# Optimization experiments

Hardware: AMD Instinct MI355X
Metric: run time of the kernel (lower is better)

## Reference

```python
import jax, jax.numpy as jnp
import numpy as np

B = 16384        # batch
P = 8            # num policies (experts)
D = 512          # latent dim
A = 64           # action dim
H = 1024         # hidden dim


def setup_inputs() -> dict:
    key = jax.random.key(0)
    ks = jax.random.split(key, 7)
    latents = jax.random.normal(ks[0], (B, D), dtype=jnp.float32)
    actions = jax.random.normal(ks[1], (B, A), dtype=jnp.float32)
    policy_indices = jax.random.randint(ks[2], (B,), 0, P, dtype=jnp.int64)
    # Per-policy 2-layer MLP params: concat(latent, action) -> hidden -> latent
    scale1 = 1.0 / np.sqrt(D + A)
    scale2 = 1.0 / np.sqrt(H)
    W1 = jax.random.normal(ks[3], (P, D + A, H), dtype=jnp.float32) * scale1
    b1 = jnp.zeros((P, H), dtype=jnp.float32)
    W2 = jax.random.normal(ks[4], (P, H, D), dtype=jnp.float32) * scale2
    b2 = jnp.zeros((P, D), dtype=jnp.float32)
    return {"latents": latents, "actions": actions, "policy_indices": policy_indices,
            "W1": W1, "b1": b1, "W2": W2, "b2": b2}


def reference(latents, actions, policy_indices, W1, b1, W2, b2):
    # Original: for each policy i, route rows with policy_indices == i through
    # that policy's dynamics model; scatter results back into next_latents.
    # Equivalent dense form: run all experts, then select per-row expert output.
    x = jnp.concatenate([latents, actions], axis=-1)          # [B, D+A]
    h = jax.nn.relu(jnp.einsum('bd,pdh->bph', x, W1) + b1)    # [B, P, H]
    y = jnp.einsum('bph,phd->bpd', h, W2) + b2                # [B, P, D]
    idx = policy_indices[:, None, None]                       # [B, 1, 1]
    next_latents = jnp.take_along_axis(y, idx, axis=1)[:, 0]  # [B, D]
    return next_latents
```

## Files before the change

kernel.cpp:

```cpp
#include <hip/hip_runtime.h>
#include <hip/hip_bf16.h>
#include <stdint.h>

#define B_SZ 16384
#define P_SZ 8
#define D_SZ 512
#define A_SZ 64
#define K1 576
#define H_SZ 1024
#define NSEG 64
#define MB_MAX 72
#define BPAD (B_SZ + P_SZ*256)
#define PREP_BLOCKS (BPAD * 72 / 256)
#define TR1_BLOCKS (P_SZ * 9 * 16)
#define TR2_BLOCKS (P_SZ * 16 * 8)
#define G1_GRID (BPAD / 128 * (H_SZ / 64))
#define G2_GRID (BPAD / 128 * (D_SZ / 64))

typedef __bf16 bf16_t;
typedef __bf16 bf16x8 __attribute__((ext_vector_type(8)));
typedef float f32x4 __attribute__((ext_vector_type(4)));

__device__ __forceinline__ void glds16(const void* g, void* l) {
    __builtin_amdgcn_global_load_lds(
        (const __attribute__((address_space(1))) unsigned*)g,
        (__attribute__((address_space(3))) unsigned*)l, 16, 0, 0);
}


__global__ __launch_bounds__(256) void hist_block(const int* __restrict__ pol,
                                                  int* __restrict__ blockhist,
                                                  int* __restrict__ rowidx) {
    __shared__ int lc[P_SZ];
    int t = threadIdx.x;
    if (t < P_SZ) lc[t] = 0;
    __syncthreads();
    int gid = blockIdx.x * 256 + t;
    rowidx[gid] = -1;
    if (gid < BPAD - B_SZ) rowidx[B_SZ + gid] = -1;
    atomicAdd(&lc[pol[gid]], 1);
    __syncthreads();
    if (t < P_SZ) blockhist[blockIdx.x * P_SZ + t] = lc[t];
}

__global__ __launch_bounds__(256) void prefix_kernel(const int* __restrict__ blockhist,
                                                     int* __restrict__ counts,
                                                     int* __restrict__ cursors,
                                                     int* __restrict__ blk_p) {
    __shared__ int csh[P_SZ];
    int t = threadIdx.x;
    int p = t >> 5, i = t & 31;
    int s = blockhist[i * P_SZ + p] + blockhist[(i + 32) * P_SZ + p];
#pragma unroll
    for (int m = 16; m >= 1; m >>= 1) s += __shfl_xor(s, m, 32);
    if (i == 0) csh[p] = s;
    __syncthreads();
    if (t == 0) {
        int run = 0;
        for (int pp = 0; pp < P_SZ; ++pp) {
            counts[pp] = csh[pp];
            cursors[pp] = run;
            run += ((csh[pp] + 255) >> 8) * 256;
        }
    }
    if (t < MB_MAX) {
        int run = 0, val = -1;
#pragma unroll
        for (int pp = 0; pp < P_SZ; ++pp) {
            int nb = (csh[pp] + 255) >> 8;
            if (t >= run && t < run + nb) val = pp;
            run += nb;
        }
        blk_p[t] = val;
    }
}

__global__ __launch_bounds__(256) void scatter_agg(const int* __restrict__ pol,
                                                   int* __restrict__ cursors,
                                                   int* __restrict__ rowidx) {
    __shared__ int lc[P_SZ], base_s[P_SZ];
    int t = threadIdx.x;
    if (t < P_SZ) lc[t] = 0;
    __syncthreads();
    int i = blockIdx.x * 256 + t;
    int p = pol[i];
    int lpos = atomicAdd(&lc[p], 1);
    __syncthreads();
    if (t < P_SZ) base_s[t] = atomicAdd(&cursors[t], lc[t]);
    __syncthreads();
    rowidx[base_s[p] + lpos] = i;
}


__global__ __launch_bounds__(256) void prep_all(const float* __restrict__ latents,
                                                const float* __restrict__ actions,
                                                const int* __restrict__ rowidx,
                                                const float* __restrict__ W1,
                                                const float* __restrict__ W2,
                                                bf16_t* __restrict__ xs,
                                                bf16_t* __restrict__ w1t,
                                                bf16_t* __restrict__ w2t) {
    int bx = blockIdx.x;
    int tid = threadIdx.x;
    if (bx < PREP_BLOCKS) {
        int idx = bx * 256 + tid;
        int s = idx / 72;
        int col = (idx - s * 72) * 8;
        int g = rowidx[s];
        bf16x8 o;
        if (g < 0) {
            o = (bf16x8){0,0,0,0,0,0,0,0};
        } else {
            const float* src;
            if (col < D_SZ) src = latents + (size_t)g * D_SZ + col;
            else            src = actions + (size_t)g * A_SZ + (col - D_SZ);
            f32x4 v0 = *(const f32x4*)src;
            f32x4 v1 = *(const f32x4*)(src + 4);
            o[0] = (bf16_t)v0[0]; o[1] = (bf16_t)v0[1]; o[2] = (bf16_t)v0[2]; o[3] = (bf16_t)v0[3];
            o[4] = (bf16_t)v1[0]; o[5] = (bf16_t)v1[1]; o[6] = (bf16_t)v1[2]; o[7] = (bf16_t)v1[3];
        }
        *(bf16x8*)(xs + (size_t)s * K1 + col) = o;
        return;
    }
    int tz = bx - PREP_BLOCKS;
    const float* Wp; bf16_t* WTp; int K, N, k0, n0;
    if (tz < TR1_BLOCKS) {
        int p = tz / 144, rem = tz % 144;
        k0 = (rem / 16) * 64; n0 = (rem % 16) * 64;
        K = K1; N = H_SZ;
        Wp = W1 + (size_t)p * K1 * H_SZ;
        WTp = w1t + (size_t)p * H_SZ * K1;
    } else {
        int u = tz - TR1_BLOCKS;
        int p = u / 128, rem = u % 128;
        k0 = (rem / 8) * 64; n0 = (rem % 8) * 64;
        K = H_SZ; N = D_SZ;
        Wp = W2 + (size_t)p * H_SZ * D_SZ;
        WTp = w2t + (size_t)p * D_SZ * H_SZ;
    }
    __shared__ float ls[64][65];
#pragma unroll
    for (int e = 0; e < 4; ++e) {
        int idx = e * 256 + tid;
        int kk = idx >> 4, nn = (idx & 15) * 4;
        f32x4 v = *(const f32x4*)&Wp[(size_t)(k0 + kk) * N + n0 + nn];
        ls[kk][nn]     = v[0];
        ls[kk][nn + 1] = v[1];
        ls[kk][nn + 2] = v[2];
        ls[kk][nn + 3] = v[3];
    }
    __syncthreads();
#pragma unroll
    for (int e = 0; e < 2; ++e) {
        int idx = e * 256 + tid;
        int nn = idx >> 3, ks = (idx & 7) * 8;
        bf16x8 o;
#pragma unroll
        for (int q = 0; q < 8; ++q) o[q] = (bf16_t)ls[ks + q][nn];
        *(bf16x8*)&WTp[(size_t)(n0 + nn) * K + k0 + ks] = o;
    }
}


__global__ __launch_bounds__(256, 6) void gemm1_kernel(
    const bf16_t* __restrict__ xs, const bf16_t* __restrict__ w1t,
    const float* __restrict__ b1, const int* __restrict__ blk_p,
    bf16_t* __restrict__ h) {

    const int b = blockIdx.x;
    const int wid = (b & 7) * (G1_GRID / 8) + (b >> 3);
    const int mb = wid >> 4;
    const int nb = wid & 15;
    const int p = blk_p[mb >> 1];
    if (p < 0) return;
    const int m0 = mb * 128;
    const int n0 = nb * 64;

    constexpr int ASUB = 128 * 32;
    constexpr int BSUB = 64 * 32;
    __shared__ __align__(16) bf16_t As[2 * ASUB];
    __shared__ __align__(16) bf16_t Bs[2 * BSUB];

    const int tid = threadIdx.x;
    const int wave = tid >> 6, lane = tid & 63;

    const bf16_t *a_src[2][2]; bf16_t *a_dst[2][2];
#pragma unroll
    for (int hh = 0; hh < 2; ++hh)
#pragma unroll
        for (int i = 0; i < 2; ++i) {
            int c = (wave * 2 + i) * 64 + lane;
            int r = c >> 2;
            int kl = (c & 3) ^ ((r >> 1) & 3);
            a_src[hh][i] = xs + (size_t)(m0 + r) * K1 + hh * 32 + kl * 8;
            a_dst[hh][i] = As + hh * ASUB + c * 8;
        }
    const bf16_t *b_src[2]; bf16_t *b_dst[2];
#pragma unroll
    for (int hh = 0; hh < 2; ++hh) {
        int c = wave * 64 + lane;
        int r = c >> 2;
        int kl = (c & 3) ^ ((r >> 1) & 3);
        b_src[hh] = w1t + ((size_t)p * H_SZ + n0 + r) * K1 + hh * 32 + kl * 8;
        b_dst[hh] = Bs + hh * BSUB + c * 8;
    }

    const int l16 = lane & 15, qd = lane >> 4;
    const int swz = (l16 >> 1) & 3;
    const int wr = wave >> 1, wc = wave & 1;
    int aoff[4], boff[2];
#pragma unroll
    for (int i = 0; i < 4; ++i) aoff[i] = (wr * 64 + i * 16 + l16) * 32 + ((qd ^ swz) * 8);
#pragma unroll
    for (int j = 0; j < 2; ++j) boff[j] = (wc * 32 + j * 16 + l16) * 32 + ((qd ^ swz) * 8);

    f32x4 acc[4][2];
#pragma unroll
    for (int i = 0; i < 4; ++i)
#pragma unroll
        for (int j = 0; j < 2; ++j)
            acc[i][j] = (f32x4){0.f, 0.f, 0.f, 0.f};

    for (int kt = 0; kt < K1; kt += 64) {
        __syncthreads();
#pragma unroll
        for (int hh = 0; hh < 2; ++hh) {
#pragma unroll
            for (int i = 0; i < 2; ++i) glds16(a_src[hh][i] + kt, a_dst[hh][i]);
            glds16(b_src[hh] + kt, b_dst[hh]);
        }
        __syncthreads();
#pragma unroll
        for (int hh = 0; hh < 2; ++hh) {
            bf16x8 af[4], bfv[2];
#pragma unroll
            for (int i = 0; i < 4; ++i) af[i] = *(const bf16x8*)(As + hh * ASUB + aoff[i]);
#pragma unroll
            for (int j = 0; j < 2; ++j) bfv[j] = *(const bf16x8*)(Bs + hh * BSUB + boff[j]);
#pragma unroll
            for (int i = 0; i < 4; ++i)
#pragma unroll
                for (int j = 0; j < 2; ++j)
                    acc[i][j] = __builtin_amdgcn_mfma_f32_16x16x32_bf16(af[i], bfv[j], acc[i][j], 0, 0, 0);
        }
    }

#pragma unroll
    for (int i = 0; i < 4; ++i) {
#pragma unroll
        for (int r = 0; r < 4; ++r) {
            int ml = wr * 64 + i * 16 + qd * 4 + r;
            size_t row = (size_t)(m0 + ml);
#pragma unroll
            for (int j = 0; j < 2; ++j) {
                int n = n0 + wc * 32 + j * 16 + l16;
                float v = acc[i][j][r] + b1[p * H_SZ + n];
                h[row * H_SZ + n] = (bf16_t)fmaxf(v, 0.f);
            }
        }
    }
}

__global__ __launch_bounds__(256, 6) void gemm2_kernel(
    const bf16_t* __restrict__ h, const bf16_t* __restrict__ w2t,
    const float* __restrict__ b2, const int* __restrict__ blk_p,
    const int* __restrict__ rowidx, float* __restrict__ out) {

    const int b = blockIdx.x;
    const int wid = (b & 7) * (G2_GRID / 8) + (b >> 3);
    const int mb = wid >> 3;
    const int nb = wid & 7;
    const int p = blk_p[mb >> 1];
    if (p < 0) return;
    const int m0 = mb * 128;
    const int n0 = nb * 64;

    constexpr int ASUB = 128 * 32;
    constexpr int BSUB = 64 * 32;
    __shared__ __align__(16) bf16_t As[2 * ASUB];
    __shared__ __align__(16) bf16_t Bs[2 * BSUB];

    const int tid = threadIdx.x;
    const int wave = tid >> 6, lane = tid & 63;

    const bf16_t *a_src[2][2]; bf16_t *a_dst[2][2];
#pragma unroll
    for (int hh = 0; hh < 2; ++hh)
#pragma unroll
        for (int i = 0; i < 2; ++i) {
            int c = (wave * 2 + i) * 64 + lane;
            int r = c >> 2;
            int kl = (c & 3) ^ ((r >> 1) & 3);
            a_src[hh][i] = h + (size_t)(m0 + r) * H_SZ + hh * 32 + kl * 8;
            a_dst[hh][i] = As + hh * ASUB + c * 8;
        }
    const bf16_t *b_src[2]; bf16_t *b_dst[2];
#pragma unroll
    for (int hh = 0; hh < 2; ++hh) {
        int c = wave * 64 + lane;
        int r = c >> 2;
        int kl = (c & 3) ^ ((r >> 1) & 3);
        b_src[hh] = w2t + ((size_t)p * D_SZ + n0 + r) * H_SZ + hh * 32 + kl * 8;
        b_dst[hh] = Bs + hh * BSUB + c * 8;
    }

    const int l16 = lane & 15, qd = lane >> 4;
    const int swz = (l16 >> 1) & 3;
    const int wr = wave >> 1, wc = wave & 1;
    int aoff[4], boff[2];
#pragma unroll
    for (int i = 0; i < 4; ++i) aoff[i] = (wr * 64 + i * 16 + l16) * 32 + ((qd ^ swz) * 8);
#pragma unroll
    for (int j = 0; j < 2; ++j) boff[j] = (wc * 32 + j * 16 + l16) * 32 + ((qd ^ swz) * 8);

    f32x4 acc[4][2];
#pragma unroll
    for (int i = 0; i < 4; ++i)
#pragma unroll
        for (int j = 0; j < 2; ++j)
            acc[i][j] = (f32x4){0.f, 0.f, 0.f, 0.f};

    for (int kt = 0; kt < H_SZ; kt += 64) {
        __syncthreads();
#pragma unroll
        for (int hh = 0; hh < 2; ++hh) {
#pragma unroll
            for (int i = 0; i < 2; ++i) glds16(a_src[hh][i] + kt, a_dst[hh][i]);
            glds16(b_src[hh] + kt, b_dst[hh]);
        }
        __syncthreads();
#pragma unroll
        for (int hh = 0; hh < 2; ++hh) {
            bf16x8 af[4], bfv[2];
#pragma unroll
            for (int i = 0; i < 4; ++i) af[i] = *(const bf16x8*)(As + hh * ASUB + aoff[i]);
#pragma unroll
            for (int j = 0; j < 2; ++j) bfv[j] = *(const bf16x8*)(Bs + hh * BSUB + boff[j]);
#pragma unroll
            for (int i = 0; i < 4; ++i)
#pragma unroll
                for (int j = 0; j < 2; ++j)
                    acc[i][j] = __builtin_amdgcn_mfma_f32_16x16x32_bf16(af[i], bfv[j], acc[i][j], 0, 0, 0);
        }
    }

#pragma unroll
    for (int i = 0; i < 4; ++i) {
#pragma unroll
        for (int r = 0; r < 4; ++r) {
            int ml = wr * 64 + i * 16 + qd * 4 + r;
            int g = rowidx[m0 + ml];
            if (g >= 0) {
                size_t orow = (size_t)g * D_SZ;
#pragma unroll
                for (int j = 0; j < 2; ++j) {
                    int n = n0 + wc * 32 + j * 16 + l16;
                    out[orow + n] = acc[i][j][r] + b2[p * D_SZ + n];
                }
            }
        }
    }
}


extern "C" void kernel_launch(void* const* d_in, const int* in_sizes, int n_in,
                              void* d_out, int out_size, void* d_ws, size_t ws_size,
                              hipStream_t stream) {
    const float* latents = (const float*)d_in[0];
    const float* actions = (const float*)d_in[1];
    const int*   pol     = (const int*)d_in[2];
    const float* W1      = (const float*)d_in[3];
    const float* b1      = (const float*)d_in[4];
    const float* W2      = (const float*)d_in[5];
    const float* b2      = (const float*)d_in[6];
    float* out = (float*)d_out;

    char* ws = (char*)d_ws;
    int* counts    = (int*)ws;
    int* cursors   = counts + P_SZ;
    int* blk_p     = cursors + P_SZ;
    int* blockhist = blk_p + MB_MAX;
    int* rowidx    = blockhist + NSEG * P_SZ;
    size_t pos = ((size_t)(2 * P_SZ + MB_MAX + NSEG * P_SZ + BPAD) * sizeof(int) + 255) & ~(size_t)255;
    bf16_t* xs  = (bf16_t*)(ws + pos);  pos += (size_t)BPAD * K1 * 2;
    bf16_t* hbuf= (bf16_t*)(ws + pos);  pos += (size_t)BPAD * H_SZ * 2;
    bf16_t* w1t = (bf16_t*)(ws + pos);  pos += (size_t)P_SZ * H_SZ * K1 * 2;
    bf16_t* w2t = (bf16_t*)(ws + pos);  pos += (size_t)P_SZ * D_SZ * H_SZ * 2;

    hist_block<<<NSEG, 256, 0, stream>>>(pol, blockhist, rowidx);
    prefix_kernel<<<1, 256, 0, stream>>>(blockhist, counts, cursors, blk_p);
    scatter_agg<<<NSEG, 256, 0, stream>>>(pol, cursors, rowidx);
    prep_all<<<PREP_BLOCKS + TR1_BLOCKS + TR2_BLOCKS, 256, 0, stream>>>(
        latents, actions, rowidx, W1, W2, xs, w1t, w2t);
    gemm1_kernel<<<G1_GRID, 256, 0, stream>>>(xs, w1t, b1, blk_p, hbuf);
    gemm2_kernel<<<G2_GRID, 256, 0, stream>>>(hbuf, w2t, b2, blk_p, rowidx, out);
}
```

Before: 194.7 us.

## Fuse row gather and bf16 conversion of inputs into gemm1 A-tile loads

Drops the separate gather/convert pass that wrote a sorted bf16 copy of latents+actions. gemm1 now loads fp32 rows straight from latents/actions through rowidx into LDS with direct global-to-LDS loads and converts to bf16 when building MFMA fragments. The intent is to remove the round trip through the xs workspace and the prep work. In exchange, each gemm1 block re-reads fp32 A data, twice the bytes of bf16, for each of the 16 N tiles. LDS for A doubles, and occupancy is lowered from 6 to 4 blocks per SM.

Result: slower. 222.7 us (+14.4%).

```diff
diff --git a/kernel.cpp b/kernel.cpp
--- a/kernel.cpp
+++ b/kernel.cpp
@@ -11,7 +11,6 @@
 #define NSEG 64
 #define MB_MAX 72
 #define BPAD (B_SZ + P_SZ*256)
-#define PREP_BLOCKS (BPAD * 72 / 256)
 #define TR1_BLOCKS (P_SZ * 9 * 16)
 #define TR2_BLOCKS (P_SZ * 16 * 8)
 #define G1_GRID (BPAD / 128 * (H_SZ / 64))
@@ -92,37 +91,12 @@
 }
 
 
-__global__ __launch_bounds__(256) void prep_all(const float* __restrict__ latents,
-                                                const float* __restrict__ actions,
-                                                const int* __restrict__ rowidx,
-                                                const float* __restrict__ W1,
-                                                const float* __restrict__ W2,
-                                                bf16_t* __restrict__ xs,
-                                                bf16_t* __restrict__ w1t,
-                                                bf16_t* __restrict__ w2t) {
-    int bx = blockIdx.x;
+__global__ __launch_bounds__(256) void prep_w(const float* __restrict__ W1,
+                                              const float* __restrict__ W2,
+                                              bf16_t* __restrict__ w1t,
+                                              bf16_t* __restrict__ w2t) {
+    int tz = blockIdx.x;
     int tid = threadIdx.x;
-    if (bx < PREP_BLOCKS) {
-        int idx = bx * 256 + tid;
-        int s = idx / 72;
-        int col = (idx - s * 72) * 8;
-        int g = rowidx[s];
-        bf16x8 o;
-        if (g < 0) {
-            o = (bf16x8){0,0,0,0,0,0,0,0};
-        } else {
-            const float* src;
-            if (col < D_SZ) src = latents + (size_t)g * D_SZ + col;
-            else            src = actions + (size_t)g * A_SZ + (col - D_SZ);
-            f32x4 v0 = *(const f32x4*)src;
-            f32x4 v1 = *(const f32x4*)(src + 4);
-            o[0] = (bf16_t)v0[0]; o[1] = (bf16_t)v0[1]; o[2] = (bf16_t)v0[2]; o[3] = (bf16_t)v0[3];
-            o[4] = (bf16_t)v1[0]; o[5] = (bf16_t)v1[1]; o[6] = (bf16_t)v1[2]; o[7] = (bf16_t)v1[3];
-        }
-        *(bf16x8*)(xs + (size_t)s * K1 + col) = o;
-        return;
-    }
-    int tz = bx - PREP_BLOCKS;
     const float* Wp; bf16_t* WTp; int K, N, k0, n0;
     if (tz < TR1_BLOCKS) {
         int p = tz / 144, rem = tz % 144;
@@ -162,8 +136,9 @@
 }
 
 
-__global__ __launch_bounds__(256, 6) void gemm1_kernel(
-    const bf16_t* __restrict__ xs, const bf16_t* __restrict__ w1t,
+__global__ __launch_bounds__(256, 4) void gemm1_kernel(
+    const float* __restrict__ latents, const float* __restrict__ actions,
+    const int* __restrict__ rowidx, const bf16_t* __restrict__ w1t,
     const float* __restrict__ b1, const int* __restrict__ blk_p,
     bf16_t* __restrict__ h) {
 
@@ -178,24 +153,24 @@
 
     constexpr int ASUB = 128 * 32;
     constexpr int BSUB = 64 * 32;
-    __shared__ __align__(16) bf16_t As[2 * ASUB];
+    __shared__ __align__(16) float  As[2 * ASUB];
     __shared__ __align__(16) bf16_t Bs[2 * BSUB];
 
     const int tid = threadIdx.x;
     const int wave = tid >> 6, lane = tid & 63;
 
-    const bf16_t *a_src[2][2]; bf16_t *a_dst[2][2];
-#pragma unroll
-    for (int hh = 0; hh < 2; ++hh)
-#pragma unroll
-        for (int i = 0; i < 2; ++i) {
-            int c = (wave * 2 + i) * 64 + lane;
-            int r = c >> 2;
-            int kl = (c & 3) ^ ((r >> 1) & 3);
-            a_src[hh][i] = xs + (size_t)(m0 + r) * K1 + hh * 32 + kl * 8;
-            a_dst[hh][i] = As + hh * ASUB + c * 8;
-        }
-    const bf16_t *b_src[2]; bf16_t *b_dst[2];
+    const float* a_lat[4]; const float* a_act[4]; float* a_dst[4];
+#pragma unroll
+    for (int ss = 0; ss < 4; ++ss) {
+        int c = (wave * 4 + ss) * 64 + lane;
+        int r = c >> 3;
+        int kc = (c & 7) ^ (r & 7);
+        int g = rowidx[m0 + r]; if (g < 0) g = 0;
+        a_lat[ss] = latents + (size_t)g * D_SZ + kc * 4;
+        a_act[ss] = actions + (size_t)g * A_SZ + kc * 4;
+        a_dst[ss] = As + c * 4;
+    }
+    const bf16_t* b_src[2]; bf16_t* b_dst[2];
 #pragma unroll
     for (int hh = 0; hh < 2; ++hh) {
         int c = wave * 64 + lane;
@@ -206,13 +181,18 @@
     }
 
     const int l16 = lane & 15, qd = lane >> 4;
-    const int swz = (l16 >> 1) & 3;
+    const int bswz = (l16 >> 1) & 3;
+    const int akey = l16 & 7;
     const int wr = wave >> 1, wc = wave & 1;
-    int aoff[4], boff[2];
-#pragma unroll
-    for (int i = 0; i < 4; ++i) aoff[i] = (wr * 64 + i * 16 + l16) * 32 + ((qd ^ swz) * 8);
-#pragma unroll
-    for (int j = 0; j < 2; ++j) boff[j] = (wc * 32 + j * 16 + l16) * 32 + ((qd ^ swz) * 8);
+    int aoff0[4], aoff1[4], boff[2];
+#pragma unroll
+    for (int i = 0; i < 4; ++i) {
+        int row = wr * 64 + i * 16 + l16;
+        aoff0[i] = row * 32 + (((2 * qd)     ^ akey) * 4);
+        aoff1[i] = row * 32 + (((2 * qd + 1) ^ akey) * 4);
+    }
+#pragma unroll
+    for (int j = 0; j < 2; ++j) boff[j] = (wc * 32 + j * 16 + l16) * 32 + ((qd ^ bswz) * 8);
 
     f32x4 acc[4][2];
 #pragma unroll
@@ -221,20 +201,33 @@
         for (int j = 0; j < 2; ++j)
             acc[i][j] = (f32x4){0.f, 0.f, 0.f, 0.f};
 
-    for (int kt = 0; kt < K1; kt += 64) {
+    for (int t = 0; t < 9; ++t) {
         __syncthreads();
+        const bool act = (t == 8);
+        const int k0 = t * 64;
 #pragma unroll
         for (int hh = 0; hh < 2; ++hh) {
 #pragma unroll
-            for (int i = 0; i < 2; ++i) glds16(a_src[hh][i] + kt, a_dst[hh][i]);
-            glds16(b_src[hh] + kt, b_dst[hh]);
+            for (int ss = 0; ss < 4; ++ss) {
+                const float* s = act ? (a_act[ss] + hh * 32)
+                                     : (a_lat[ss] + k0 + hh * 32);
+                glds16(s, a_dst[ss] + hh * ASUB);
+            }
+            glds16(b_src[hh] + k0, b_dst[hh]);
         }
         __syncthreads();
 #pragma unroll
         for (int hh = 0; hh < 2; ++hh) {
-            bf16x8 af[4], bfv[2];
-#pragma unroll
-            for (int i = 0; i < 4; ++i) af[i] = *(const bf16x8*)(As + hh * ASUB + aoff[i]);
+            bf16x8 af[4]; bf16x8 bfv[2];
+#pragma unroll
+            for (int i = 0; i < 4; ++i) {
+                f32x4 lo = *(const f32x4*)(As + hh * ASUB + aoff0[i]);
+                f32x4 hi = *(const f32x4*)(As + hh * ASUB + aoff1[i]);
+                af[i][0] = (bf16_t)lo[0]; af[i][1] = (bf16_t)lo[1];
+                af[i][2] = (bf16_t)lo[2]; af[i][3] = (bf16_t)lo[3];
+                af[i][4] = (bf16_t)hi[0]; af[i][5] = (bf16_t)hi[1];
+                af[i][6] = (bf16_t)hi[2]; af[i][7] = (bf16_t)hi[3];
+            }
 #pragma unroll
             for (int j = 0; j < 2; ++j) bfv[j] = *(const bf16x8*)(Bs + hh * BSUB + boff[j]);
 #pragma unroll
@@ -382,7 +375,6 @@
     int* blockhist = blk_p + MB_MAX;
     int* rowidx    = blockhist + NSEG * P_SZ;
     size_t pos = ((size_t)(2 * P_SZ + MB_MAX + NSEG * P_SZ + BPAD) * sizeof(int) + 255) & ~(size_t)255;
-    bf16_t* xs  = (bf16_t*)(ws + pos);  pos += (size_t)BPAD * K1 * 2;
     bf16_t* hbuf= (bf16_t*)(ws + pos);  pos += (size_t)BPAD * H_SZ * 2;
     bf16_t* w1t = (bf16_t*)(ws + pos);  pos += (size_t)P_SZ * H_SZ * K1 * 2;
     bf16_t* w2t = (bf16_t*)(ws + pos);  pos += (size_t)P_SZ * D_SZ * H_SZ * 2;
@@ -390,8 +382,7 @@
     hist_block<<<NSEG, 256, 0, stream>>>(pol, blockhist, rowidx);
     prefix_kernel<<<1, 256, 0, stream>>>(blockhist, counts, cursors, blk_p);
     scatter_agg<<<NSEG, 256, 0, stream>>>(pol, cursors, rowidx);
-    prep_all<<<PREP_BLOCKS + TR1_BLOCKS + TR2_BLOCKS, 256, 0, stream>>>(
-        latents, actions, rowidx, W1, W2, xs, w1t, w2t);
-    gemm1_kernel<<<G1_GRID, 256, 0, stream>>>(xs, w1t, b1, blk_p, hbuf);
+    prep_w<<<TR1_BLOCKS + TR2_BLOCKS, 256, 0, stream>>>(W1, W2, w1t, w2t);
+    gemm1_kernel<<<G1_GRID, 256, 0, stream>>>(latents, actions, rowidx, w1t, b1, blk_p, hbuf);
     gemm2_kernel<<<G2_GRID, 256, 0, stream>>>(hbuf, w2t, b2, blk_p, rowidx, out);
 }
```
